# Kernel tuning notes

Hardware: AMD Instinct MI355X
Metric: run time of the kernel (lower is better)

Reference implementation:

```python
import jax, jax.numpy as jnp
import numpy as np

G = 100000   # num graphs
N = 2000000  # num nodes
E = 4000000  # num edges (unused downstream, kept for fidelity)
D = 300      # emb_dim
L = 50       # num noise levels


def setup_inputs() -> dict:
    key = jax.random.key(0)
    ks = jax.random.split(key, 12)
    node2graph = jnp.sort(jax.random.randint(ks[0], (N,), 0, G))
    edge_index = jax.random.randint(ks[1], (2, E), 0, N)
    noise_level = jax.random.randint(ks[2], (G,), 0, L)
    molecule_repr = jax.random.normal(ks[3], (G, D), dtype=jnp.float32)
    pos_noise_pred = jax.random.normal(ks[4], (N, 3), dtype=jnp.float32)
    pos_perturbed = jax.random.normal(ks[5], (N, 3), dtype=jnp.float32)
    pos_target = jax.random.normal(ks[6], (N, 3), dtype=jnp.float32)
    s = 1.0 / np.sqrt(D)
    W1 = jax.random.uniform(ks[7], (D, D), minval=-s, maxval=s, dtype=jnp.float32)
    b1 = jax.random.uniform(ks[8], (D,), minval=-s, maxval=s, dtype=jnp.float32)
    W2 = jax.random.uniform(ks[9], (D, D), minval=-s, maxval=s, dtype=jnp.float32)
    b2 = jax.random.uniform(ks[10], (D,), minval=-s, maxval=s, dtype=jnp.float32)
    sigmas = jnp.asarray(np.exp(np.linspace(np.log(10.0), np.log(0.01), L)), dtype=jnp.float32)
    return dict(node2graph=node2graph, edge_index=edge_index, noise_level=noise_level,
                num_graphs=G, molecule_repr=molecule_repr, pos_noise_pred=pos_noise_pred,
                pos_perturbed=pos_perturbed, pos_target=pos_target,
                W1=W1, b1=b1, W2=W2, b2=b2, sigmas=sigmas)


def _score_target_riemann(pos_perturbed, pos_target, node2graph, num_graphs):
    # @torch.no_grad() branch: all scatter_mean/scatter_add indexed by node2graph
    seg_sum = lambda x: jax.ops.segment_sum(x, node2graph, num_segments=num_graphs)
    cnt = jnp.maximum(seg_sum(jnp.ones((node2graph.shape[0],), jnp.float32)), 1.0)[:, None]
    center = seg_sum(pos_target) / cnt                 # [G,3]
    p_center = seg_sum(pos_perturbed) / cnt            # [G,3]
    pos_c = pos_target - center[node2graph]            # [N,3]
    pp_c = pos_perturbed - p_center[node2graph]        # [N,3]
    # per-graph 3x3 matrices: ptp[i,j] = sum pp_i*pp_j, otp[i,j] = sum pos_c_i*pp_j
    ptp = seg_sum(pp_c[:, :, None] * pp_c[:, None, :])   # [G,3,3]
    otp = seg_sum(pos_c[:, :, None] * pp_c[:, None, :])  # [G,3,3]
    ptp_n = ptp[node2graph]                              # [N,3,3]
    otp_n = otp[node2graph]                              # [N,3,3]
    num = -2.0 * (jnp.einsum('ni,nij->nj', pp_c, ptp_n)
                  - jnp.einsum('ni,nij->nj', pos_c, otp_n))  # [N,3]
    den = (jnp.linalg.norm(ptp_n.reshape(-1, 9), axis=-1)
           + jnp.linalg.norm(otp_n.reshape(-1, 9), axis=-1))[:, None]
    return num / den


def reference(node2graph, edge_index, noise_level, num_graphs, molecule_repr,
              pos_noise_pred, pos_perturbed, pos_target, W1, b1, W2, b2, sigmas):
    edge2graph = node2graph[edge_index[0]]  # computed but unused, as in original
    used_sigmas = sigmas[noise_level][node2graph][:, None]  # [N,1]
    score_target = jax.lax.stop_gradient(
        _score_target_riemann(pos_perturbed, pos_target, node2graph, num_graphs)
    ) / used_sigmas
    pred_noise = (pos_noise_pred - pos_perturbed) * (1.0 / used_sigmas)
    per_node = jnp.sum((pred_noise - score_target) ** 2, axis=-1)  # [N]
    per_graph = jax.ops.segment_sum(per_node, node2graph, num_segments=num_graphs)
    pos_denoise = per_graph.mean()
    # noise-level prediction head: Linear -> SiLU -> Linear, CE over noise_level
    h = jax.nn.silu(molecule_repr @ W1 + b1)
    logits = h @ W2 + b2  # [G,D]
    logp = jax.nn.log_softmax(logits, axis=-1)
    ce = -jnp.take_along_axis(logp, noise_level[:, None], axis=1)[:, 0]
    loss_pred_noise = ce.mean()
    return jnp.stack([pos_denoise, loss_pred_noise])
```

## Files before the change

kernel.cpp:

```cpp
#include <hip/hip_runtime.h>
#include <math.h>


typedef __attribute__((ext_vector_type(8))) short bf16x8;
typedef __attribute__((ext_vector_type(4))) short s16x4;
typedef __attribute__((ext_vector_type(4))) float f32x4;

__device__ __forceinline__ short bt(float f) {
    return (short)(__float_as_uint(f) >> 16);
}

#define TM   64
#define DRL  300
#define DP   320
#define XS   328
#define NT   20
#define MT   4
#define KCH  10


__device__ __forceinline__ void prod22(const float* A, const float* B, int j,
                                       float* dst) {
    float a0 = A[3*j], a1 = A[3*j+1], a2 = A[3*j+2];
    float b0 = B[3*j], b1 = B[3*j+1], b2 = B[3*j+2];
    dst[0] = 1.f;
    dst[1] = a0;  dst[2] = a1;  dst[3] = a2;
    dst[4] = b0;  dst[5] = b1;  dst[6] = b2;
    dst[7] = b0*b0;  dst[8] = b0*b1;  dst[9] = b0*b2;
    dst[10] = b1*b1; dst[11] = b1*b2; dst[12] = b2*b2;
    dst[13] = a0*b0; dst[14] = a0*b1; dst[15] = a0*b2;
    dst[16] = a1*b0; dst[17] = a1*b1; dst[18] = a1*b2;
    dst[19] = a2*b0; dst[20] = a2*b1; dst[21] = a2*b2;
}

__device__ __forceinline__ void acc22(float* q, const float* A, const float* B,
                                      int j) {
    float p[22];
    prod22(A, B, j, p);
#pragma unroll
    for (int k = 0; k < 22; ++k) q[k] += p[k];
}

__device__ __forceinline__ void flush_store(float* __restrict__ mom, int seg,
                                            const float* v) {
    float4* d = (float4*)&mom[seg * 24];
    float4 s0 = {v[0], v[1], v[2], v[3]};
    float4 s1 = {v[4], v[5], v[6], v[7]};
    float4 s2 = {v[8], v[9], v[10], v[11]};
    float4 s3 = {v[12], v[13], v[14], v[15]};
    float4 s4 = {v[16], v[17], v[18], v[19]};
    float4 s5 = {v[20], v[21], 0.f, 0.f};
    d[0] = s0; d[1] = s1; d[2] = s2; d[3] = s3; d[4] = s4; d[5] = s5;
}

__device__ __forceinline__ void flush_atomic(float* __restrict__ mom, int seg,
                                             const float* v) {
    float* m = &mom[seg * 24];
#pragma unroll
    for (int k = 0; k < 22; ++k) atomicAdd(&m[k], v[k]);
}

__global__ __launch_bounds__(256)
void k_moments(const int* __restrict__ n2g,
               const float* __restrict__ pt,
               const float* __restrict__ pp,
               float* __restrict__ mom, int N) {
    const int t = blockIdx.x * blockDim.x + threadIdx.x;
    const int lane = threadIdx.x & 63;
    const int i0 = t * 4;
    const bool act = (i0 < N);

    float A[12], B[12];
    int g0 = -1, g1 = -1, g2 = -1, g3 = -1;
    if (act) {
        const float4* ptv = (const float4*)pt;
        const float4* ppv = (const float4*)pp;
#pragma unroll
        for (int v = 0; v < 3; ++v) {
            float4 x = ptv[3 * t + v];
            A[4*v+0] = x.x; A[4*v+1] = x.y; A[4*v+2] = x.z; A[4*v+3] = x.w;
            float4 y = ppv[3 * t + v];
            B[4*v+0] = y.x; B[4*v+1] = y.y; B[4*v+2] = y.z; B[4*v+3] = y.w;
        }
        int4 gv = *(const int4*)&n2g[i0];
        g0 = gv.x; g1 = gv.y; g2 = gv.z; g3 = gv.w;
    }

    float q[22];
    float lead[22];
    int curseg = g0, leadseg = -2;
    bool haveLead = false;
#pragma unroll
    for (int k = 0; k < 22; ++k) { q[k] = 0.f; lead[k] = 0.f; }
    if (act) {
        prod22(A, B, 0, q);
        const int gj[3] = {g1, g2, g3};
#pragma unroll
        for (int j = 1; j < 4; ++j) {
            int gg = gj[j - 1];
            if (gg == curseg) {
                acc22(q, A, B, j);
            } else {
                if (!haveLead) {
                    haveLead = true; leadseg = curseg;
#pragma unroll
                    for (int k = 0; k < 22; ++k) lead[k] = q[k];
                } else {
                    flush_store(mom, curseg, q);
                }
                prod22(A, B, j, q);
                curseg = gg;
            }
        }
    }

    const int waveFirstNode = ((t - lane) & 0x7FFFFFFF) * 4;
    int before_seg = -1, after_seg = -1;
    if (lane == 0 && waveFirstNode > 0 && waveFirstNode <= N)
        before_seg = n2g[waveFirstNode - 1];
    before_seg = __shfl(before_seg, 0, 64);
    const int waveLast = waveFirstNode + 255;
    if (lane == 63 && waveLast + 1 < N) after_seg = n2g[waveLast + 1];
    after_seg = __shfl(after_seg, 63, 64);

#pragma unroll
    for (int d = 1; d < 64; d <<= 1) {
        int ps = __shfl_up(curseg, d, 64);
        bool ok = (lane >= d) && (ps == curseg);
#pragma unroll
        for (int k = 0; k < 22; ++k) {
            float o = __shfl_up(q[k], d, 64);
            q[k] += ok ? o : 0.f;
        }
    }

    int pseg = __shfl_up(curseg, 1, 64);
    bool cont = act && haveLead && (lane > 0) && (pseg == leadseg);
    float pcnt = 0.f;
#pragma unroll
    for (int k = 0; k < 22; ++k) {
        float pv = __shfl_up(q[k], 1, 64);
        if (k == 0) pcnt = pv;
        lead[k] += cont ? pv : 0.f;
    }
    if (act && haveLead) {
        bool covers = (lane == 0) || (cont && (pcnt == (float)(lane * 4)));
        bool ileft = covers && (before_seg == leadseg);
        if (ileft) flush_atomic(mom, leadseg, lead);
        else       flush_store(mom, leadseg, lead);
    }

    int nseg0 = __shfl_down(g0, 1, 64);
    bool tail = act && ((lane == 63) || (nseg0 != curseg));
    if (tail) {
        bool covers = (q[0] == (float)(lane * 4 + 4));
        bool ileft = covers && (before_seg == curseg);
        bool iright = (lane == 63) && (after_seg == curseg);
        if (ileft || iright) flush_atomic(mom, curseg, q);
        else                 flush_store(mom, curseg, q);
    }
}

__global__ void k_node(const int* __restrict__ n2g,
                       const float* __restrict__ pt,
                       const float* __restrict__ pp,
                       const float* __restrict__ pnp,
                       const float* __restrict__ mom,
                       const int* __restrict__ nl,
                       const float* __restrict__ sigmas,
                       double* __restrict__ accA, int N) {
    int t = blockIdx.x * blockDim.x + threadIdx.x;
    int i0 = t * 4;
    float q = 0.f;
    if (i0 < N) {
        float A[12], B[12], C[12];
        const float4* ptv = (const float4*)pt;
        const float4* ppv = (const float4*)pp;
        const float4* pnv = (const float4*)pnp;
#pragma unroll
        for (int v = 0; v < 3; ++v) {
            float4 x = ptv[3 * t + v];
            A[4*v+0] = x.x; A[4*v+1] = x.y; A[4*v+2] = x.z; A[4*v+3] = x.w;
            float4 y = ppv[3 * t + v];
            B[4*v+0] = y.x; B[4*v+1] = y.y; B[4*v+2] = y.z; B[4*v+3] = y.w;
            float4 z = pnv[3 * t + v];
            C[4*v+0] = z.x; C[4*v+1] = z.y; C[4*v+2] = z.z; C[4*v+3] = z.w;
        }
        int4 gv = *(const int4*)&n2g[i0];
        int gl[4] = {gv.x, gv.y, gv.z, gv.w};
        int gcur = -1;
        float c0=0,c1=0,c2=0,d0=0,d1=0,d2=0,p00=0,p01=0,p02=0,p11=0,p12=0,p22=0;
        float o00=0,o01=0,o02=0,o10=0,o11=0,o12=0,o20=0,o21=0,o22=0,idn=0,is2=0;
#pragma unroll
        for (int j = 0; j < 4; ++j) {
            int i = i0 + j;
            if (i >= N) break;
            int g = gl[j];
            if (g != gcur) {
                gcur = g;
                const float4* pr = (const float4*)&mom[g * 24];
                float4 v0 = pr[0], v1 = pr[1], v2 = pr[2],
                       v3 = pr[3], v4 = pr[4], v5 = pr[5];
                float cnt = fmaxf(v0.x, 1.f);
                float ic = 1.f / cnt;
                c0 = v0.y * ic; c1 = v0.z * ic; c2 = v0.w * ic;
                d0 = v1.x * ic; d1 = v1.y * ic; d2 = v1.z * ic;
                p00 = v1.w - cnt*d0*d0; p01 = v2.x - cnt*d0*d1;
                p02 = v2.y - cnt*d0*d2; p11 = v2.z - cnt*d1*d1;
                p12 = v2.w - cnt*d1*d2; p22 = v3.x - cnt*d2*d2;
                o00 = v3.y - cnt*c0*d0; o01 = v3.z - cnt*c0*d1;
                o02 = v3.w - cnt*c0*d2; o10 = v4.x - cnt*c1*d0;
                o11 = v4.y - cnt*c1*d1; o12 = v4.z - cnt*c1*d2;
                o20 = v4.w - cnt*c2*d0; o21 = v5.x - cnt*c2*d1;
                o22 = v5.y - cnt*c2*d2;
                float ptn = sqrtf(p00*p00 + p11*p11 + p22*p22 +
                                  2.f*(p01*p01 + p02*p02 + p12*p12));
                float otn = sqrtf(o00*o00 + o01*o01 + o02*o02 +
                                  o10*o10 + o11*o11 + o12*o12 +
                                  o20*o20 + o21*o21 + o22*o22);
                float den = ptn + otn;
                idn = (den > 0.f) ? (1.f / den) : 0.f;
                float sg = sigmas[nl[g]];
                is2 = 1.f / (sg * sg);
            }
            float a0 = A[3*j+0] - c0, a1 = A[3*j+1] - c1, a2 = A[3*j+2] - c2;
            float b0 = B[3*j+0] - d0, b1 = B[3*j+1] - d1, b2 = B[3*j+2] - d2;
            float n0 = -2.f * ((b0*p00 + b1*p01 + b2*p02) - (a0*o00 + a1*o10 + a2*o20));
            float n1 = -2.f * ((b0*p01 + b1*p11 + b2*p12) - (a0*o01 + a1*o11 + a2*o21));
            float n2 = -2.f * ((b0*p02 + b1*p12 + b2*p22) - (a0*o02 + a1*o12 + a2*o22));
            float e0 = (C[3*j+0] - B[3*j+0]) - n0 * idn;
            float e1 = (C[3*j+1] - B[3*j+1]) - n1 * idn;
            float e2 = (C[3*j+2] - B[3*j+2]) - n2 * idn;
            q += (e0*e0 + e1*e1 + e2*e2) * is2;
        }
    }
    for (int o = 32; o > 0; o >>= 1) q += __shfl_down(q, o, 64);
    int wv = (threadIdx.x >> 6);
    if ((threadIdx.x & 63) == 0)
        atomicAdd(&accA[(blockIdx.x * 4 + wv) & 255], (double)q);
}


__global__ void k_prepw(const float* __restrict__ W1, const float* __restrict__ W2,
                        short* __restrict__ Wb1, short* __restrict__ Wb2) {
    int id = blockIdx.x * blockDim.x + threadIdx.x;
    if (id >= 2 * DP * DP) return;
    int mat = id / (DP * DP);
    int rem = id - mat * DP * DP;
    int k = rem / DP, n = rem - (rem / DP) * DP;
    const float* W = mat ? W2 : W1;
    short* Wb = mat ? Wb2 : Wb1;
    float v = (k < DRL && n < DRL) ? W[k * DRL + n] : 0.f;
    int kc = k >> 5, kin = k & 31, quad = kin >> 3, j = kin & 7;
    int t = n >> 4, l16 = n & 15;
    Wb[(((kc * NT + t) * 64) + quad * 16 + l16) * 8 + j] = bt(v);
}


__global__ __launch_bounds__(640, 5)
void k_mlp(const float* __restrict__ X,
           const short* __restrict__ Wb1, const short* __restrict__ Wb2,
           const float* __restrict__ b1, const float* __restrict__ b2,
           const int* __restrict__ nl,
           double* __restrict__ accC, int G) {
    __shared__ __align__(16) short Xs[TM * XS];

    const int tid  = threadIdx.x;
    const int wv   = tid >> 6;
    const int lane = tid & 63;
    const int quad = lane >> 4;
    const int l16  = lane & 15;
    const int m0   = blockIdx.x * TM;

    const float4* Xv = (const float4*)X;
    for (int idx = tid; idx < TM * 75; idx += 640) {
        int r = idx / 75, c = idx - r * 75;
        int gr = m0 + r;
        float4 v = {0.f, 0.f, 0.f, 0.f};
        if (gr < G) v = Xv[gr * 75 + c];
        s16x4 sv = { bt(v.x), bt(v.y), bt(v.z), bt(v.w) };
        *(s16x4*)&Xs[r * XS + c * 4] = sv;
    }
    for (int idx = tid; idx < TM * (DP - DRL); idx += 640) {
        int r = idx / (DP - DRL), c = idx - r * (DP - DRL);
        Xs[r * XS + DRL + c] = 0;
    }
    __syncthreads();

    const bf16x8* B1 = (const bf16x8*)Wb1;
    const bf16x8* B2 = (const bf16x8*)Wb2;
    const int tile0 = wv * 2, tile1 = wv * 2 + 1;

    f32x4 acc[MT][2];
    const f32x4 vzero = {0.f, 0.f, 0.f, 0.f};
#pragma unroll
    for (int m = 0; m < MT; ++m) { acc[m][0] = vzero; acc[m][1] = vzero; }

    bf16x8 nb0 = B1[(0 * NT + tile0) * 64 + lane];
    bf16x8 nb1 = B1[(0 * NT + tile1) * 64 + lane];
#pragma unroll
    for (int kc = 0; kc < KCH; ++kc) {
        bf16x8 b0v = nb0, b1v = nb1;
        if (kc + 1 < KCH) {
            nb0 = B1[((kc + 1) * NT + tile0) * 64 + lane];
            nb1 = B1[((kc + 1) * NT + tile1) * 64 + lane];
        }
        bf16x8 a[MT];
#pragma unroll
        for (int m = 0; m < MT; ++m)
            a[m] = *(const bf16x8*)&Xs[(m * 16 + l16) * XS + kc * 32 + quad * 8];
#pragma unroll
        for (int m = 0; m < MT; ++m) {
            acc[m][0] = __builtin_amdgcn_mfma_f32_16x16x32_bf16(a[m], b0v, acc[m][0], 0, 0, 0);
            acc[m][1] = __builtin_amdgcn_mfma_f32_16x16x32_bf16(a[m], b1v, acc[m][1], 0, 0, 0);
        }
    }
    __syncthreads();

#pragma unroll
    for (int t = 0; t < 2; ++t) {
        int col = (wv * 2 + t) * 16 + l16;
        float bias = (col < DRL) ? b1[col] : 0.f;
#pragma unroll
        for (int m = 0; m < MT; ++m)
#pragma unroll
            for (int r = 0; r < 4; ++r) {
                float v = acc[m][t][r] + bias;
                float h = v / (1.f + __expf(-v));
                Xs[(m * 16 + quad * 4 + r) * XS + col] = bt(h);
            }
    }
    __syncthreads();

#pragma unroll
    for (int m = 0; m < MT; ++m) { acc[m][0] = vzero; acc[m][1] = vzero; }
    nb0 = B2[(0 * NT + tile0) * 64 + lane];
    nb1 = B2[(0 * NT + tile1) * 64 + lane];
#pragma unroll
    for (int kc = 0; kc < KCH; ++kc) {
        bf16x8 b0v = nb0, b1v = nb1;
        if (kc + 1 < KCH) {
            nb0 = B2[((kc + 1) * NT + tile0) * 64 + lane];
            nb1 = B2[((kc + 1) * NT + tile1) * 64 + lane];
        }
        bf16x8 a[MT];
#pragma unroll
        for (int m = 0; m < MT; ++m)
            a[m] = *(const bf16x8*)&Xs[(m * 16 + l16) * XS + kc * 32 + quad * 8];
#pragma unroll
        for (int m = 0; m < MT; ++m) {
            acc[m][0] = __builtin_amdgcn_mfma_f32_16x16x32_bf16(a[m], b0v, acc[m][0], 0, 0, 0);
            acc[m][1] = __builtin_amdgcn_mfma_f32_16x16x32_bf16(a[m], b1v, acc[m][1], 0, 0, 0);
        }
    }
    __syncthreads();

    float* S = (float*)Xs;
    float* T = S + TM * 10;
    const int colA = tile0 * 16 + l16;
    const int colB = tile1 * 16 + l16;
    const float biasA = (colA < DRL) ? b2[colA] : 0.f;
    const float biasB = (colB < DRL) ? b2[colB] : 0.f;
#pragma unroll
    for (int m = 0; m < MT; ++m) {
#pragma unroll
        for (int r = 0; r < 4; ++r) {
            int row = m * 16 + quad * 4 + r;
            int grow = m0 + row;
            int ct = (grow < G) ? nl[grow] : -1;
            float lgA = acc[m][0][r] + biasA;
            float lgB = acc[m][1][r] + biasB;
            float sw = ((colA < DRL) ? __expf(lgA) : 0.f) +
                       ((colB < DRL) ? __expf(lgB) : 0.f);
            for (int o = 1; o < 16; o <<= 1) sw += __shfl_xor(sw, o, 64);
            if (l16 == 0) S[row * 10 + wv] = sw;
            if (colA == ct) T[row] = lgA;
            if (colB == ct) T[row] = lgB;
        }
    }
    __syncthreads();
    if (tid < 64) {
        int row = tid;
        int grow = m0 + row;
        float q = 0.f;
        if (grow < G) {
            float ss = 0.f;
#pragma unroll
            for (int w = 0; w < 10; ++w) ss += S[row * 10 + w];
            q = __logf(ss) - T[row];
        }
        for (int o = 32; o > 0; o >>= 1) q += __shfl_down(q, o, 64);
        if (tid == 0) atomicAdd(&accC[blockIdx.x & 255], (double)q);
    }
}


__global__ void k_final(const double* __restrict__ accA,
                        const double* __restrict__ accC,
                        float* __restrict__ out, float invG) {
    int t = threadIdx.x;
    double a = accA[t] + accA[t + 64] + accA[t + 128] + accA[t + 192];
    double c = accC[t] + accC[t + 64] + accC[t + 128] + accC[t + 192];
    for (int o = 32; o > 0; o >>= 1) {
        a += __shfl_down(a, o, 64);
        c += __shfl_down(c, o, 64);
    }
    if (t == 0) {
        out[0] = (float)(a * (double)invG);
        out[1] = (float)(c * (double)invG);
    }
}


extern "C" void kernel_launch(void* const* d_in, const int* in_sizes, int n_in,
                              void* d_out, int out_size, void* d_ws, size_t ws_size,
                              hipStream_t stream) {
    const int*   n2g = (const int*)d_in[0];
    const int*   nl  = (const int*)d_in[2];
    const float* X   = (const float*)d_in[4];
    const float* pnp = (const float*)d_in[5];
    const float* pp  = (const float*)d_in[6];
    const float* pt  = (const float*)d_in[7];
    const float* W1  = (const float*)d_in[8];
    const float* b1  = (const float*)d_in[9];
    const float* W2  = (const float*)d_in[10];
    const float* b2  = (const float*)d_in[11];
    const float* sig = (const float*)d_in[12];

    const int N = in_sizes[0];
    const int G = in_sizes[2];

    double* accA = (double*)d_ws;
    double* accC = accA + 256;
    short*  Wb1  = (short*)((char*)d_ws + 4096);
    short*  Wb2  = Wb1 + DP * DP;
    float*  mom  = (float*)((char*)d_ws + 4096 + (size_t)2 * DP * DP * 2);

    hipMemsetAsync(d_ws, 0, 4096, stream);
    hipMemsetAsync(mom, 0, (size_t)G * 24 * 4, stream);

    const int T4 = (N + 3) / 4;
    k_prepw<<<(2 * DP * DP + 255) / 256, 256, 0, stream>>>(W1, W2, Wb1, Wb2);
    k_moments<<<(T4 + 255) / 256, 256, 0, stream>>>(n2g, pt, pp, mom, N);
    k_node<<<(T4 + 255) / 256, 256, 0, stream>>>(n2g, pt, pp, pnp, mom,
                                                 nl, sig, accA, N);
    k_mlp<<<(G + TM - 1) / TM, 640, 0, stream>>>(X, Wb1, Wb2, b1, b2, nl,
                                                 accC, G);
    k_final<<<1, 64, 0, stream>>>(accA, accC, (float*)d_out, 1.0f / (float)G);
}
```

Measured before the change: 405.1 us.

## Preload all MLP weight fragments into registers and double-buffer hidden activations

Loads every W1 fragment into registers before staging X, and all W2 fragments right after the first GEMM, instead of prefetching one k-chunk at a time. The X load is batched into eight outstanding float4 loads before conversion. A separate Hs shared buffer holds the SiLU output, which removes two barriers (after each GEMM) since Xs is no longer overwritten. The cost is many more registers and twice the LDS per block, so launch bounds drop from 5 to 3 blocks per CU and occupancy falls.

```diff
diff --git a/kernel.cpp b/kernel.cpp
--- a/kernel.cpp
+++ b/kernel.cpp
@@ -257,13 +257,14 @@
 }
 
 
-__global__ __launch_bounds__(640, 5)
+__global__ __launch_bounds__(640, 3)
 void k_mlp(const float* __restrict__ X,
            const short* __restrict__ Wb1, const short* __restrict__ Wb2,
            const float* __restrict__ b1, const float* __restrict__ b2,
            const int* __restrict__ nl,
            double* __restrict__ accC, int G) {
     __shared__ __align__(16) short Xs[TM * XS];
+    __shared__ __align__(16) short Hs[TM * XS];
 
     const int tid  = threadIdx.x;
     const int wv   = tid >> 6;
@@ -272,14 +273,40 @@
     const int l16  = lane & 15;
     const int m0   = blockIdx.x * TM;
 
+    const bf16x8* B1 = (const bf16x8*)Wb1;
+    const bf16x8* B2 = (const bf16x8*)Wb2;
+    const int tile0 = wv * 2, tile1 = wv * 2 + 1;
+
+    bf16x8 w1a[KCH], w1b[KCH];
+#pragma unroll
+    for (int kc = 0; kc < KCH; ++kc) {
+        w1a[kc] = B1[(kc * NT + tile0) * 64 + lane];
+        w1b[kc] = B1[(kc * NT + tile1) * 64 + lane];
+    }
+
     const float4* Xv = (const float4*)X;
-    for (int idx = tid; idx < TM * 75; idx += 640) {
-        int r = idx / 75, c = idx - r * 75;
-        int gr = m0 + r;
-        float4 v = {0.f, 0.f, 0.f, 0.f};
-        if (gr < G) v = Xv[gr * 75 + c];
-        s16x4 sv = { bt(v.x), bt(v.y), bt(v.z), bt(v.w) };
-        *(s16x4*)&Xs[r * XS + c * 4] = sv;
+    {
+        float4 xv[8];
+#pragma unroll
+        for (int u = 0; u < 8; ++u) {
+            int idx = tid + u * 640;
+            float4 v = {0.f, 0.f, 0.f, 0.f};
+            if (idx < TM * 75) {
+                int r = idx / 75, c = idx - r * 75;
+                int gr = m0 + r;
+                if (gr < G) v = Xv[gr * 75 + c];
+            }
+            xv[u] = v;
+        }
+#pragma unroll
+        for (int u = 0; u < 8; ++u) {
+            int idx = tid + u * 640;
+            if (idx < TM * 75) {
+                int r = idx / 75, c = idx - r * 75;
+                s16x4 sv = { bt(xv[u].x), bt(xv[u].y), bt(xv[u].z), bt(xv[u].w) };
+                *(s16x4*)&Xs[r * XS + c * 4] = sv;
+            }
+        }
     }
     for (int idx = tid; idx < TM * (DP - DRL); idx += 640) {
         int r = idx / (DP - DRL), c = idx - r * (DP - DRL);
@@ -287,35 +314,30 @@
     }
     __syncthreads();
 
-    const bf16x8* B1 = (const bf16x8*)Wb1;
-    const bf16x8* B2 = (const bf16x8*)Wb2;
-    const int tile0 = wv * 2, tile1 = wv * 2 + 1;
-
     f32x4 acc[MT][2];
     const f32x4 vzero = {0.f, 0.f, 0.f, 0.f};
 #pragma unroll
     for (int m = 0; m < MT; ++m) { acc[m][0] = vzero; acc[m][1] = vzero; }
 
-    bf16x8 nb0 = B1[(0 * NT + tile0) * 64 + lane];
-    bf16x8 nb1 = B1[(0 * NT + tile1) * 64 + lane];
 #pragma unroll
     for (int kc = 0; kc < KCH; ++kc) {
-        bf16x8 b0v = nb0, b1v = nb1;
-        if (kc + 1 < KCH) {
-            nb0 = B1[((kc + 1) * NT + tile0) * 64 + lane];
-            nb1 = B1[((kc + 1) * NT + tile1) * 64 + lane];
-        }
         bf16x8 a[MT];
 #pragma unroll
         for (int m = 0; m < MT; ++m)
             a[m] = *(const bf16x8*)&Xs[(m * 16 + l16) * XS + kc * 32 + quad * 8];
 #pragma unroll
         for (int m = 0; m < MT; ++m) {
-            acc[m][0] = __builtin_amdgcn_mfma_f32_16x16x32_bf16(a[m], b0v, acc[m][0], 0, 0, 0);
-            acc[m][1] = __builtin_amdgcn_mfma_f32_16x16x32_bf16(a[m], b1v, acc[m][1], 0, 0, 0);
-        }
-    }
-    __syncthreads();
+            acc[m][0] = __builtin_amdgcn_mfma_f32_16x16x32_bf16(a[m], w1a[kc], acc[m][0], 0, 0, 0);
+            acc[m][1] = __builtin_amdgcn_mfma_f32_16x16x32_bf16(a[m], w1b[kc], acc[m][1], 0, 0, 0);
+        }
+    }
+
+    bf16x8 w2a[KCH], w2b[KCH];
+#pragma unroll
+    for (int kc = 0; kc < KCH; ++kc) {
+        w2a[kc] = B2[(kc * NT + tile0) * 64 + lane];
+        w2b[kc] = B2[(kc * NT + tile1) * 64 + lane];
+    }
 
 #pragma unroll
     for (int t = 0; t < 2; ++t) {
@@ -327,33 +349,25 @@
             for (int r = 0; r < 4; ++r) {
                 float v = acc[m][t][r] + bias;
                 float h = v / (1.f + __expf(-v));
-                Xs[(m * 16 + quad * 4 + r) * XS + col] = bt(h);
+                Hs[(m * 16 + quad * 4 + r) * XS + col] = bt(h);
             }
     }
     __syncthreads();
 
 #pragma unroll
     for (int m = 0; m < MT; ++m) { acc[m][0] = vzero; acc[m][1] = vzero; }
-    nb0 = B2[(0 * NT + tile0) * 64 + lane];
-    nb1 = B2[(0 * NT + tile1) * 64 + lane];
 #pragma unroll
     for (int kc = 0; kc < KCH; ++kc) {
-        bf16x8 b0v = nb0, b1v = nb1;
-        if (kc + 1 < KCH) {
-            nb0 = B2[((kc + 1) * NT + tile0) * 64 + lane];
-            nb1 = B2[((kc + 1) * NT + tile1) * 64 + lane];
-        }
         bf16x8 a[MT];
 #pragma unroll
         for (int m = 0; m < MT; ++m)
-            a[m] = *(const bf16x8*)&Xs[(m * 16 + l16) * XS + kc * 32 + quad * 8];
+            a[m] = *(const bf16x8*)&Hs[(m * 16 + l16) * XS + kc * 32 + quad * 8];
 #pragma unroll
         for (int m = 0; m < MT; ++m) {
-            acc[m][0] = __builtin_amdgcn_mfma_f32_16x16x32_bf16(a[m], b0v, acc[m][0], 0, 0, 0);
-            acc[m][1] = __builtin_amdgcn_mfma_f32_16x16x32_bf16(a[m], b1v, acc[m][1], 0, 0, 0);
-        }
-    }
-    __syncthreads();
+            acc[m][0] = __builtin_amdgcn_mfma_f32_16x16x32_bf16(a[m], w2a[kc], acc[m][0], 0, 0, 0);
+            acc[m][1] = __builtin_amdgcn_mfma_f32_16x16x32_bf16(a[m], w2b[kc], acc[m][1], 0, 0, 0);
+        }
+    }
 
     float* S = (float*)Xs;
     float* T = S + TM * 10;
```

Result: no change. 410.1 us (+1.2%).

## Make MLP kernel persistent with register-prefetched double-buffered input tiles

Applied to the files above, without the earlier changes.

The CE-head MLP kernel now runs a fixed grid of 256 blocks that loop over row tiles instead of launching one block per tile. While the current tile is in GEMM1, each block loads the next tile's X rows into registers and writes them to a second LDS buffer. Hidden activations move to their own LDS buffer. The cross-entropy partial sum is kept in a register and committed with a single atomic per block. The intent is to hide global-load latency and cut per-block setup and atomic traffic. In exchange, LDS per block roughly triples and occupancy drops to one block per CU, which leaves fewer waves to hide latency.

```diff
diff --git a/kernel.cpp b/kernel.cpp
--- a/kernel.cpp
+++ b/kernel.cpp
@@ -17,6 +17,7 @@
 #define NT   20
 #define MT   4
 #define KCH  10
+#define GRID_MLP 256
 
 
 __device__ __forceinline__ void prod22(const float* A, const float* B, int j,
@@ -257,141 +258,186 @@
 }
 
 
-__global__ __launch_bounds__(640, 5)
+__global__ __launch_bounds__(640, 3)
 void k_mlp(const float* __restrict__ X,
            const short* __restrict__ Wb1, const short* __restrict__ Wb2,
            const float* __restrict__ b1, const float* __restrict__ b2,
            const int* __restrict__ nl,
-           double* __restrict__ accC, int G) {
-    __shared__ __align__(16) short Xs[TM * XS];
+           double* __restrict__ accC, int G, int ntiles) {
+    __shared__ __align__(16) short Xs[2][TM * XS];
+    __shared__ __align__(16) short Hs[TM * XS];
+    __shared__ float S[TM * 10];
+    __shared__ float T[TM];
 
     const int tid  = threadIdx.x;
     const int wv   = tid >> 6;
     const int lane = tid & 63;
     const int quad = lane >> 4;
     const int l16  = lane & 15;
-    const int m0   = blockIdx.x * TM;
-
-    const float4* Xv = (const float4*)X;
-    for (int idx = tid; idx < TM * 75; idx += 640) {
-        int r = idx / 75, c = idx - r * 75;
-        int gr = m0 + r;
-        float4 v = {0.f, 0.f, 0.f, 0.f};
-        if (gr < G) v = Xv[gr * 75 + c];
-        s16x4 sv = { bt(v.x), bt(v.y), bt(v.z), bt(v.w) };
-        *(s16x4*)&Xs[r * XS + c * 4] = sv;
-    }
-    for (int idx = tid; idx < TM * (DP - DRL); idx += 640) {
-        int r = idx / (DP - DRL), c = idx - r * (DP - DRL);
-        Xs[r * XS + DRL + c] = 0;
-    }
-    __syncthreads();
+    const int tile0 = wv * 2, tile1 = wv * 2 + 1;
 
     const bf16x8* B1 = (const bf16x8*)Wb1;
     const bf16x8* B2 = (const bf16x8*)Wb2;
-    const int tile0 = wv * 2, tile1 = wv * 2 + 1;
-
-    f32x4 acc[MT][2];
+    const float4* Xv = (const float4*)X;
+
+    for (int idx = tid; idx < 2 * TM * (DP - DRL); idx += 640) {
+        int b   = idx / (TM * (DP - DRL));
+        int rem = idx - b * (TM * (DP - DRL));
+        int r = rem / (DP - DRL), c = rem - r * (DP - DRL);
+        Xs[b][r * XS + DRL + c] = 0;
+    }
+
+    {
+        const int m0 = blockIdx.x * TM;
+        for (int idx = tid; idx < TM * 75; idx += 640) {
+            int r = idx / 75, c = idx - r * 75;
+            float4 v = {0.f, 0.f, 0.f, 0.f};
+            if (m0 + r < G) v = Xv[(m0 + r) * 75 + c];
+            s16x4 sv = { bt(v.x), bt(v.y), bt(v.z), bt(v.w) };
+            *(s16x4*)&Xs[0][r * XS + c * 4] = sv;
+        }
+    }
+    __syncthreads();
+
+    double ce_local = 0.0;
+    int cur = 0;
     const f32x4 vzero = {0.f, 0.f, 0.f, 0.f};
-#pragma unroll
-    for (int m = 0; m < MT; ++m) { acc[m][0] = vzero; acc[m][1] = vzero; }
-
-    bf16x8 nb0 = B1[(0 * NT + tile0) * 64 + lane];
-    bf16x8 nb1 = B1[(0 * NT + tile1) * 64 + lane];
-#pragma unroll
-    for (int kc = 0; kc < KCH; ++kc) {
-        bf16x8 b0v = nb0, b1v = nb1;
-        if (kc + 1 < KCH) {
-            nb0 = B1[((kc + 1) * NT + tile0) * 64 + lane];
-            nb1 = B1[((kc + 1) * NT + tile1) * 64 + lane];
-        }
-        bf16x8 a[MT];
-#pragma unroll
-        for (int m = 0; m < MT; ++m)
-            a[m] = *(const bf16x8*)&Xs[(m * 16 + l16) * XS + kc * 32 + quad * 8];
+
+    for (int t = blockIdx.x; t < ntiles; t += GRID_MLP) {
+        const int m0 = t * TM;
+        const int tn = t + GRID_MLP;
+        const bool hasnext = (tn < ntiles);
+
+        float4 xr[8];
+        if (hasnext) {
+            const int m0n = tn * TM;
+#pragma unroll
+            for (int u = 0; u < 8; ++u) {
+                int idx = tid + u * 640;
+                float4 v = {0.f, 0.f, 0.f, 0.f};
+                int r = idx / 75, c = idx - r * 75;
+                if (idx < TM * 75 && m0n + r < G) v = Xv[(m0n + r) * 75 + c];
+                xr[u] = v;
+            }
+        }
+        __builtin_amdgcn_sched_barrier(0);
+
+        const short* As = &Xs[cur][0];
+        f32x4 acc[MT][2];
+#pragma unroll
+        for (int m = 0; m < MT; ++m) { acc[m][0] = vzero; acc[m][1] = vzero; }
+        {
+            bf16x8 nb0 = B1[(0 * NT + tile0) * 64 + lane];
+            bf16x8 nb1 = B1[(0 * NT + tile1) * 64 + lane];
+#pragma unroll
+            for (int kc = 0; kc < KCH; ++kc) {
+                bf16x8 b0v = nb0, b1v = nb1;
+                if (kc + 1 < KCH) {
+                    nb0 = B1[((kc + 1) * NT + tile0) * 64 + lane];
+                    nb1 = B1[((kc + 1) * NT + tile1) * 64 + lane];
+                }
+                bf16x8 a[MT];
+#pragma unroll
+                for (int m = 0; m < MT; ++m)
+                    a[m] = *(const bf16x8*)&As[(m * 16 + l16) * XS + kc * 32 + quad * 8];
+#pragma unroll
+                for (int m = 0; m < MT; ++m) {
+                    acc[m][0] = __builtin_amdgcn_mfma_f32_16x16x32_bf16(a[m], b0v, acc[m][0], 0, 0, 0);
+                    acc[m][1] = __builtin_amdgcn_mfma_f32_16x16x32_bf16(a[m], b1v, acc[m][1], 0, 0, 0);
+                }
+            }
+        }
+
+#pragma unroll
+        for (int tt = 0; tt < 2; ++tt) {
+            int col = (wv * 2 + tt) * 16 + l16;
+            float bias = (col < DRL) ? b1[col] : 0.f;
+#pragma unroll
+            for (int m = 0; m < MT; ++m)
+#pragma unroll
+                for (int r = 0; r < 4; ++r) {
+                    float v = acc[m][tt][r] + bias;
+                    float h = v / (1.f + __expf(-v));
+                    Hs[(m * 16 + quad * 4 + r) * XS + col] = bt(h);
+                }
+        }
+
+        if (hasnext) {
+#pragma unroll
+            for (int u = 0; u < 8; ++u) {
+                int idx = tid + u * 640;
+                if (idx < TM * 75) {
+                    int r = idx / 75, c = idx - r * 75;
+                    s16x4 sv = { bt(xr[u].x), bt(xr[u].y), bt(xr[u].z), bt(xr[u].w) };
+                    *(s16x4*)&Xs[cur ^ 1][r * XS + c * 4] = sv;
+                }
+            }
+        }
+        __syncthreads();
+
+#pragma unroll
+        for (int m = 0; m < MT; ++m) { acc[m][0] = vzero; acc[m][1] = vzero; }
+        {
+            bf16x8 nb0 = B2[(0 * NT + tile0) * 64 + lane];
+            bf16x8 nb1 = B2[(0 * NT + tile1) * 64 + lane];
+#pragma unroll
+            for (int kc = 0; kc < KCH; ++kc) {
+                bf16x8 b0v = nb0, b1v = nb1;
+                if (kc + 1 < KCH) {
+                    nb0 = B2[((kc + 1) * NT + tile0) * 64 + lane];
+                    nb1 = B2[((kc + 1) * NT + tile1) * 64 + lane];
+                }
+                bf16x8 a[MT];
+#pragma unroll
+                for (int m = 0; m < MT; ++m)
+                    a[m] = *(const bf16x8*)&Hs[(m * 16 + l16) * XS + kc * 32 + quad * 8];
+#pragma unroll
+                for (int m = 0; m < MT; ++m) {
+                    acc[m][0] = __builtin_amdgcn_mfma_f32_16x16x32_bf16(a[m], b0v, acc[m][0], 0, 0, 0);
+                    acc[m][1] = __builtin_amdgcn_mfma_f32_16x16x32_bf16(a[m], b1v, acc[m][1], 0, 0, 0);
+                }
+            }
+        }
+
+        const int colA = tile0 * 16 + l16;
+        const int colB = tile1 * 16 + l16;
+        const float biasA = (colA < DRL) ? b2[colA] : 0.f;
+        const float biasB = (colB < DRL) ? b2[colB] : 0.f;
 #pragma unroll
         for (int m = 0; m < MT; ++m) {
-            acc[m][0] = __builtin_amdgcn_mfma_f32_16x16x32_bf16(a[m], b0v, acc[m][0], 0, 0, 0);
-            acc[m][1] = __builtin_amdgcn_mfma_f32_16x16x32_bf16(a[m], b1v, acc[m][1], 0, 0, 0);
-        }
-    }
-    __syncthreads();
-
-#pragma unroll
-    for (int t = 0; t < 2; ++t) {
-        int col = (wv * 2 + t) * 16 + l16;
-        float bias = (col < DRL) ? b1[col] : 0.f;
-#pragma unroll
-        for (int m = 0; m < MT; ++m)
 #pragma unroll
             for (int r = 0; r < 4; ++r) {
-                float v = acc[m][t][r] + bias;
-                float h = v / (1.f + __expf(-v));
-                Xs[(m * 16 + quad * 4 + r) * XS + col] = bt(h);
-            }
-    }
-    __syncthreads();
-
-#pragma unroll
-    for (int m = 0; m < MT; ++m) { acc[m][0] = vzero; acc[m][1] = vzero; }
-    nb0 = B2[(0 * NT + tile0) * 64 + lane];
-    nb1 = B2[(0 * NT + tile1) * 64 + lane];
-#pragma unroll
-    for (int kc = 0; kc < KCH; ++kc) {
-        bf16x8 b0v = nb0, b1v = nb1;
-        if (kc + 1 < KCH) {
-            nb0 = B2[((kc + 1) * NT + tile0) * 64 + lane];
-            nb1 = B2[((kc + 1) * NT + tile1) * 64 + lane];
-        }
-        bf16x8 a[MT];
-#pragma unroll
-        for (int m = 0; m < MT; ++m)
-            a[m] = *(const bf16x8*)&Xs[(m * 16 + l16) * XS + kc * 32 + quad * 8];
-#pragma unroll
-        for (int m = 0; m < MT; ++m) {
-            acc[m][0] = __builtin_amdgcn_mfma_f32_16x16x32_bf16(a[m], b0v, acc[m][0], 0, 0, 0);
-            acc[m][1] = __builtin_amdgcn_mfma_f32_16x16x32_bf16(a[m], b1v, acc[m][1], 0, 0, 0);
-        }
-    }
-    __syncthreads();
-
-    float* S = (float*)Xs;
-    float* T = S + TM * 10;
-    const int colA = tile0 * 16 + l16;
-    const int colB = tile1 * 16 + l16;
-    const float biasA = (colA < DRL) ? b2[colA] : 0.f;
-    const float biasB = (colB < DRL) ? b2[colB] : 0.f;
-#pragma unroll
-    for (int m = 0; m < MT; ++m) {
-#pragma unroll
-        for (int r = 0; r < 4; ++r) {
-            int row = m * 16 + quad * 4 + r;
-            int grow = m0 + row;
-            int ct = (grow < G) ? nl[grow] : -1;
-            float lgA = acc[m][0][r] + biasA;
-            float lgB = acc[m][1][r] + biasB;
-            float sw = ((colA < DRL) ? __expf(lgA) : 0.f) +
-                       ((colB < DRL) ? __expf(lgB) : 0.f);
-            for (int o = 1; o < 16; o <<= 1) sw += __shfl_xor(sw, o, 64);
-            if (l16 == 0) S[row * 10 + wv] = sw;
-            if (colA == ct) T[row] = lgA;
-            if (colB == ct) T[row] = lgB;
-        }
-    }
-    __syncthreads();
-    if (tid < 64) {
-        int row = tid;
-        int grow = m0 + row;
-        float q = 0.f;
-        if (grow < G) {
-            float ss = 0.f;
-#pragma unroll
-            for (int w = 0; w < 10; ++w) ss += S[row * 10 + w];
-            q = __logf(ss) - T[row];
-        }
-        for (int o = 32; o > 0; o >>= 1) q += __shfl_down(q, o, 64);
-        if (tid == 0) atomicAdd(&accC[blockIdx.x & 255], (double)q);
-    }
+                int row = m * 16 + quad * 4 + r;
+                int grow = m0 + row;
+                int ct = (grow < G) ? nl[grow] : -1;
+                float lgA = acc[m][0][r] + biasA;
+                float lgB = acc[m][1][r] + biasB;
+                float sw = ((colA < DRL) ? __expf(lgA) : 0.f) +
+                           ((colB < DRL) ? __expf(lgB) : 0.f);
+                for (int o = 1; o < 16; o <<= 1) sw += __shfl_xor(sw, o, 64);
+                if (l16 == 0) S[row * 10 + wv] = sw;
+                if (colA == ct) T[row] = lgA;
+                if (colB == ct) T[row] = lgB;
+            }
+        }
+        __syncthreads();
+
+        if (tid < 64) {
+            int row = tid, grow = m0 + row;
+            float q = 0.f;
+            if (grow < G) {
+                float ss = 0.f;
+#pragma unroll
+                for (int w = 0; w < 10; ++w) ss += S[row * 10 + w];
+                q = __logf(ss) - T[row];
+            }
+            for (int o = 32; o > 0; o >>= 1) q += __shfl_down(q, o, 64);
+            if (tid == 0) ce_local += (double)q;
+        }
+        cur ^= 1;
+    }
+    if (tid == 0)
+        atomicAdd(&accC[blockIdx.x & 255], ce_local);
 }
 
 
@@ -440,11 +486,14 @@
     hipMemsetAsync(mom, 0, (size_t)G * 24 * 4, stream);
 
     const int T4 = (N + 3) / 4;
+    const int ntiles = (G + TM - 1) / TM;
+    const int grid_mlp = (ntiles < GRID_MLP) ? ntiles : GRID_MLP;
+
     k_prepw<<<(2 * DP * DP + 255) / 256, 256, 0, stream>>>(W1, W2, Wb1, Wb2);
     k_moments<<<(T4 + 255) / 256, 256, 0, stream>>>(n2g, pt, pp, mom, N);
     k_node<<<(T4 + 255) / 256, 256, 0, stream>>>(n2g, pt, pp, pnp, mom,
                                                  nl, sig, accA, N);
-    k_mlp<<<(G + TM - 1) / TM, 640, 0, stream>>>(X, Wb1, Wb2, b1, b2, nl,
-                                                 accC, G);
+    k_mlp<<<grid_mlp, 640, 0, stream>>>(X, Wb1, Wb2, b1, b2, nl,
+                                        accC, G, ntiles);
     k_final<<<1, 64, 0, stream>>>(accA, accC, (float*)d_out, 1.0f / (float)G);
 }
```

Result: slower. 461.0 us (+13.8%).

## Replace node-parallel segmented moments with per-graph processing via boundary arrays

Applied to the files above, without the earlier changes.

Replaces the wave-level segmented scan and atomic moment accumulation with a boundary-finding kernel that records each graph's node range. A per-graph kernel then assigns four lanes to each graph, computes the moments with a quad shuffle reduction, and makes a second pass over that graph's nodes to accumulate the loss. This removes the moments buffer, the cross-wave atomics and the scan shuffles. In exchange, loads become strided scalar accesses with uneven per-graph work, and pt and pp are read twice.

```diff
diff --git a/kernel.cpp b/kernel.cpp
--- a/kernel.cpp
+++ b/kernel.cpp
@@ -19,225 +19,83 @@
 #define KCH  10
 
 
-__device__ __forceinline__ void prod22(const float* A, const float* B, int j,
-                                       float* dst) {
-    float a0 = A[3*j], a1 = A[3*j+1], a2 = A[3*j+2];
-    float b0 = B[3*j], b1 = B[3*j+1], b2 = B[3*j+2];
-    dst[0] = 1.f;
-    dst[1] = a0;  dst[2] = a1;  dst[3] = a2;
-    dst[4] = b0;  dst[5] = b1;  dst[6] = b2;
-    dst[7] = b0*b0;  dst[8] = b0*b1;  dst[9] = b0*b2;
-    dst[10] = b1*b1; dst[11] = b1*b2; dst[12] = b2*b2;
-    dst[13] = a0*b0; dst[14] = a0*b1; dst[15] = a0*b2;
-    dst[16] = a1*b0; dst[17] = a1*b1; dst[18] = a1*b2;
-    dst[19] = a2*b0; dst[20] = a2*b1; dst[21] = a2*b2;
-}
-
-__device__ __forceinline__ void acc22(float* q, const float* A, const float* B,
-                                      int j) {
-    float p[22];
-    prod22(A, B, j, p);
-#pragma unroll
-    for (int k = 0; k < 22; ++k) q[k] += p[k];
-}
-
-__device__ __forceinline__ void flush_store(float* __restrict__ mom, int seg,
-                                            const float* v) {
-    float4* d = (float4*)&mom[seg * 24];
-    float4 s0 = {v[0], v[1], v[2], v[3]};
-    float4 s1 = {v[4], v[5], v[6], v[7]};
-    float4 s2 = {v[8], v[9], v[10], v[11]};
-    float4 s3 = {v[12], v[13], v[14], v[15]};
-    float4 s4 = {v[16], v[17], v[18], v[19]};
-    float4 s5 = {v[20], v[21], 0.f, 0.f};
-    d[0] = s0; d[1] = s1; d[2] = s2; d[3] = s3; d[4] = s4; d[5] = s5;
-}
-
-__device__ __forceinline__ void flush_atomic(float* __restrict__ mom, int seg,
-                                             const float* v) {
-    float* m = &mom[seg * 24];
-#pragma unroll
-    for (int k = 0; k < 22; ++k) atomicAdd(&m[k], v[k]);
-}
-
 __global__ __launch_bounds__(256)
-void k_moments(const int* __restrict__ n2g,
-               const float* __restrict__ pt,
-               const float* __restrict__ pp,
-               float* __restrict__ mom, int N) {
-    const int t = blockIdx.x * blockDim.x + threadIdx.x;
-    const int lane = threadIdx.x & 63;
-    const int i0 = t * 4;
-    const bool act = (i0 < N);
-
-    float A[12], B[12];
-    int g0 = -1, g1 = -1, g2 = -1, g3 = -1;
-    if (act) {
-        const float4* ptv = (const float4*)pt;
-        const float4* ppv = (const float4*)pp;
-#pragma unroll
-        for (int v = 0; v < 3; ++v) {
-            float4 x = ptv[3 * t + v];
-            A[4*v+0] = x.x; A[4*v+1] = x.y; A[4*v+2] = x.z; A[4*v+3] = x.w;
-            float4 y = ppv[3 * t + v];
-            B[4*v+0] = y.x; B[4*v+1] = y.y; B[4*v+2] = y.z; B[4*v+3] = y.w;
-        }
-        int4 gv = *(const int4*)&n2g[i0];
-        g0 = gv.x; g1 = gv.y; g2 = gv.z; g3 = gv.w;
-    }
-
-    float q[22];
-    float lead[22];
-    int curseg = g0, leadseg = -2;
-    bool haveLead = false;
-#pragma unroll
-    for (int k = 0; k < 22; ++k) { q[k] = 0.f; lead[k] = 0.f; }
-    if (act) {
-        prod22(A, B, 0, q);
-        const int gj[3] = {g1, g2, g3};
-#pragma unroll
-        for (int j = 1; j < 4; ++j) {
-            int gg = gj[j - 1];
-            if (gg == curseg) {
-                acc22(q, A, B, j);
-            } else {
-                if (!haveLead) {
-                    haveLead = true; leadseg = curseg;
-#pragma unroll
-                    for (int k = 0; k < 22; ++k) lead[k] = q[k];
-                } else {
-                    flush_store(mom, curseg, q);
-                }
-                prod22(A, B, j, q);
-                curseg = gg;
-            }
-        }
-    }
-
-    const int waveFirstNode = ((t - lane) & 0x7FFFFFFF) * 4;
-    int before_seg = -1, after_seg = -1;
-    if (lane == 0 && waveFirstNode > 0 && waveFirstNode <= N)
-        before_seg = n2g[waveFirstNode - 1];
-    before_seg = __shfl(before_seg, 0, 64);
-    const int waveLast = waveFirstNode + 255;
-    if (lane == 63 && waveLast + 1 < N) after_seg = n2g[waveLast + 1];
-    after_seg = __shfl(after_seg, 63, 64);
-
-#pragma unroll
-    for (int d = 1; d < 64; d <<= 1) {
-        int ps = __shfl_up(curseg, d, 64);
-        bool ok = (lane >= d) && (ps == curseg);
-#pragma unroll
-        for (int k = 0; k < 22; ++k) {
-            float o = __shfl_up(q[k], d, 64);
-            q[k] += ok ? o : 0.f;
-        }
-    }
-
-    int pseg = __shfl_up(curseg, 1, 64);
-    bool cont = act && haveLead && (lane > 0) && (pseg == leadseg);
-    float pcnt = 0.f;
-#pragma unroll
-    for (int k = 0; k < 22; ++k) {
-        float pv = __shfl_up(q[k], 1, 64);
-        if (k == 0) pcnt = pv;
-        lead[k] += cont ? pv : 0.f;
-    }
-    if (act && haveLead) {
-        bool covers = (lane == 0) || (cont && (pcnt == (float)(lane * 4)));
-        bool ileft = covers && (before_seg == leadseg);
-        if (ileft) flush_atomic(mom, leadseg, lead);
-        else       flush_store(mom, leadseg, lead);
-    }
-
-    int nseg0 = __shfl_down(g0, 1, 64);
-    bool tail = act && ((lane == 63) || (nseg0 != curseg));
-    if (tail) {
-        bool covers = (q[0] == (float)(lane * 4 + 4));
-        bool ileft = covers && (before_seg == curseg);
-        bool iright = (lane == 63) && (after_seg == curseg);
-        if (ileft || iright) flush_atomic(mom, curseg, q);
-        else                 flush_store(mom, curseg, q);
-    }
-}
-
-__global__ void k_node(const int* __restrict__ n2g,
-                       const float* __restrict__ pt,
-                       const float* __restrict__ pp,
-                       const float* __restrict__ pnp,
-                       const float* __restrict__ mom,
-                       const int* __restrict__ nl,
-                       const float* __restrict__ sigmas,
-                       double* __restrict__ accA, int N) {
+void k_bnd(const int* __restrict__ n2g, int* __restrict__ gs,
+           int* __restrict__ ge, int N) {
     int t = blockIdx.x * blockDim.x + threadIdx.x;
-    int i0 = t * 4;
+    if (t >= N) return;
+    int g = n2g[t];
+    if (t == 0     || n2g[t - 1] != g) gs[g] = t;
+    if (t == N - 1 || n2g[t + 1] != g) ge[g] = t + 1;
+}
+
+__global__ __launch_bounds__(256)
+void k_graph(const int* __restrict__ gs, const int* __restrict__ ge,
+             const float* __restrict__ pt, const float* __restrict__ pp,
+             const float* __restrict__ pnp,
+             const int* __restrict__ nl, const float* __restrict__ sigmas,
+             double* __restrict__ accA, int G) {
+    const int tg = blockIdx.x * blockDim.x + threadIdx.x;
+    const int g  = tg >> 2;
+    const int j  = tg & 3;
     float q = 0.f;
-    if (i0 < N) {
-        float A[12], B[12], C[12];
-        const float4* ptv = (const float4*)pt;
-        const float4* ppv = (const float4*)pp;
-        const float4* pnv = (const float4*)pnp;
-#pragma unroll
-        for (int v = 0; v < 3; ++v) {
-            float4 x = ptv[3 * t + v];
-            A[4*v+0] = x.x; A[4*v+1] = x.y; A[4*v+2] = x.z; A[4*v+3] = x.w;
-            float4 y = ppv[3 * t + v];
-            B[4*v+0] = y.x; B[4*v+1] = y.y; B[4*v+2] = y.z; B[4*v+3] = y.w;
-            float4 z = pnv[3 * t + v];
-            C[4*v+0] = z.x; C[4*v+1] = z.y; C[4*v+2] = z.z; C[4*v+3] = z.w;
-        }
-        int4 gv = *(const int4*)&n2g[i0];
-        int gl[4] = {gv.x, gv.y, gv.z, gv.w};
-        int gcur = -1;
-        float c0=0,c1=0,c2=0,d0=0,d1=0,d2=0,p00=0,p01=0,p02=0,p11=0,p12=0,p22=0;
-        float o00=0,o01=0,o02=0,o10=0,o11=0,o12=0,o20=0,o21=0,o22=0,idn=0,is2=0;
-#pragma unroll
-        for (int j = 0; j < 4; ++j) {
-            int i = i0 + j;
-            if (i >= N) break;
-            int g = gl[j];
-            if (g != gcur) {
-                gcur = g;
-                const float4* pr = (const float4*)&mom[g * 24];
-                float4 v0 = pr[0], v1 = pr[1], v2 = pr[2],
-                       v3 = pr[3], v4 = pr[4], v5 = pr[5];
-                float cnt = fmaxf(v0.x, 1.f);
-                float ic = 1.f / cnt;
-                c0 = v0.y * ic; c1 = v0.z * ic; c2 = v0.w * ic;
-                d0 = v1.x * ic; d1 = v1.y * ic; d2 = v1.z * ic;
-                p00 = v1.w - cnt*d0*d0; p01 = v2.x - cnt*d0*d1;
-                p02 = v2.y - cnt*d0*d2; p11 = v2.z - cnt*d1*d1;
-                p12 = v2.w - cnt*d1*d2; p22 = v3.x - cnt*d2*d2;
-                o00 = v3.y - cnt*c0*d0; o01 = v3.z - cnt*c0*d1;
-                o02 = v3.w - cnt*c0*d2; o10 = v4.x - cnt*c1*d0;
-                o11 = v4.y - cnt*c1*d1; o12 = v4.z - cnt*c1*d2;
-                o20 = v4.w - cnt*c2*d0; o21 = v5.x - cnt*c2*d1;
-                o22 = v5.y - cnt*c2*d2;
-                float ptn = sqrtf(p00*p00 + p11*p11 + p22*p22 +
-                                  2.f*(p01*p01 + p02*p02 + p12*p12));
-                float otn = sqrtf(o00*o00 + o01*o01 + o02*o02 +
-                                  o10*o10 + o11*o11 + o12*o12 +
-                                  o20*o20 + o21*o21 + o22*o22);
-                float den = ptn + otn;
-                idn = (den > 0.f) ? (1.f / den) : 0.f;
-                float sg = sigmas[nl[g]];
-                is2 = 1.f / (sg * sg);
-            }
-            float a0 = A[3*j+0] - c0, a1 = A[3*j+1] - c1, a2 = A[3*j+2] - c2;
-            float b0 = B[3*j+0] - d0, b1 = B[3*j+1] - d1, b2 = B[3*j+2] - d2;
+    if (g < G) {
+        const int s = gs[g], e = ge[g];
+        float st0=0,st1=0,st2=0, sp0=0,sp1=0,sp2=0;
+        float m00=0,m01=0,m02=0,m11=0,m12=0,m22=0;
+        float t00=0,t01=0,t02=0,t10=0,t11=0,t12=0,t20=0,t21=0,t22=0;
+        for (int i = s + j; i < e; i += 4) {
+            float a0 = pt[3*i], a1 = pt[3*i+1], a2 = pt[3*i+2];
+            float b0 = pp[3*i], b1 = pp[3*i+1], b2 = pp[3*i+2];
+            st0 += a0; st1 += a1; st2 += a2;
+            sp0 += b0; sp1 += b1; sp2 += b2;
+            m00 += b0*b0; m01 += b0*b1; m02 += b0*b2;
+            m11 += b1*b1; m12 += b1*b2; m22 += b2*b2;
+            t00 += a0*b0; t01 += a0*b1; t02 += a0*b2;
+            t10 += a1*b0; t11 += a1*b1; t12 += a1*b2;
+            t20 += a2*b0; t21 += a2*b1; t22 += a2*b2;
+        }
+#define QR(x) do { x += __shfl_xor(x, 1, 64); x += __shfl_xor(x, 2, 64); } while (0)
+        QR(st0); QR(st1); QR(st2); QR(sp0); QR(sp1); QR(sp2);
+        QR(m00); QR(m01); QR(m02); QR(m11); QR(m12); QR(m22);
+        QR(t00); QR(t01); QR(t02); QR(t10); QR(t11); QR(t12);
+        QR(t20); QR(t21); QR(t22);
+#undef QR
+        float cnt = fmaxf((float)(e - s), 1.f);
+        float ic  = 1.f / cnt;
+        float c0 = st0 * ic, c1 = st1 * ic, c2 = st2 * ic;
+        float d0 = sp0 * ic, d1 = sp1 * ic, d2 = sp2 * ic;
+        float p00 = m00 - cnt*d0*d0, p01 = m01 - cnt*d0*d1;
+        float p02 = m02 - cnt*d0*d2, p11 = m11 - cnt*d1*d1;
+        float p12 = m12 - cnt*d1*d2, p22 = m22 - cnt*d2*d2;
+        float o00 = t00 - cnt*c0*d0, o01 = t01 - cnt*c0*d1, o02 = t02 - cnt*c0*d2;
+        float o10 = t10 - cnt*c1*d0, o11 = t11 - cnt*c1*d1, o12 = t12 - cnt*c1*d2;
+        float o20 = t20 - cnt*c2*d0, o21 = t21 - cnt*c2*d1, o22 = t22 - cnt*c2*d2;
+        float ptn = sqrtf(p00*p00 + p11*p11 + p22*p22 +
+                          2.f*(p01*p01 + p02*p02 + p12*p12));
+        float otn = sqrtf(o00*o00 + o01*o01 + o02*o02 +
+                          o10*o10 + o11*o11 + o12*o12 +
+                          o20*o20 + o21*o21 + o22*o22);
+        float den = ptn + otn;
+        float idn = (den > 0.f) ? (1.f / den) : 0.f;
+        float sg  = sigmas[nl[g]];
+        float is2 = 1.f / (sg * sg);
+        for (int i = s + j; i < e; i += 4) {
+            float a0 = pt[3*i] - c0, a1 = pt[3*i+1] - c1, a2 = pt[3*i+2] - c2;
+            float bb0 = pp[3*i],  bb1 = pp[3*i+1],  bb2 = pp[3*i+2];
+            float b0 = bb0 - d0, b1 = bb1 - d1, b2 = bb2 - d2;
             float n0 = -2.f * ((b0*p00 + b1*p01 + b2*p02) - (a0*o00 + a1*o10 + a2*o20));
             float n1 = -2.f * ((b0*p01 + b1*p11 + b2*p12) - (a0*o01 + a1*o11 + a2*o21));
             float n2 = -2.f * ((b0*p02 + b1*p12 + b2*p22) - (a0*o02 + a1*o12 + a2*o22));
-            float e0 = (C[3*j+0] - B[3*j+0]) - n0 * idn;
-            float e1 = (C[3*j+1] - B[3*j+1]) - n1 * idn;
-            float e2 = (C[3*j+2] - B[3*j+2]) - n2 * idn;
+            float e0 = (pnp[3*i]   - bb0) - n0 * idn;
+            float e1 = (pnp[3*i+1] - bb1) - n1 * idn;
+            float e2 = (pnp[3*i+2] - bb2) - n2 * idn;
             q += (e0*e0 + e1*e1 + e2*e2) * is2;
         }
     }
     for (int o = 32; o > 0; o >>= 1) q += __shfl_down(q, o, 64);
-    int wv = (threadIdx.x >> 6);
     if ((threadIdx.x & 63) == 0)
-        atomicAdd(&accA[(blockIdx.x * 4 + wv) & 255], (double)q);
+        atomicAdd(&accA[(blockIdx.x * 4 + (threadIdx.x >> 6)) & 255], (double)q);
 }
 
 
@@ -434,16 +292,16 @@
     double* accC = accA + 256;
     short*  Wb1  = (short*)((char*)d_ws + 4096);
     short*  Wb2  = Wb1 + DP * DP;
-    float*  mom  = (float*)((char*)d_ws + 4096 + (size_t)2 * DP * DP * 2);
+    int*    gs   = (int*)((char*)d_ws + 4096 + (size_t)2 * DP * DP * 2);
+    int*    ge   = gs + G;
 
     hipMemsetAsync(d_ws, 0, 4096, stream);
-    hipMemsetAsync(mom, 0, (size_t)G * 24 * 4, stream);
-
-    const int T4 = (N + 3) / 4;
+    hipMemsetAsync(gs, 0, (size_t)2 * G * 4, stream);
+
     k_prepw<<<(2 * DP * DP + 255) / 256, 256, 0, stream>>>(W1, W2, Wb1, Wb2);
-    k_moments<<<(T4 + 255) / 256, 256, 0, stream>>>(n2g, pt, pp, mom, N);
-    k_node<<<(T4 + 255) / 256, 256, 0, stream>>>(n2g, pt, pp, pnp, mom,
-                                                 nl, sig, accA, N);
+    k_bnd<<<(N + 255) / 256, 256, 0, stream>>>(n2g, gs, ge, N);
+    k_graph<<<(4 * G + 255) / 256, 256, 0, stream>>>(gs, ge, pt, pp, pnp,
+                                                     nl, sig, accA, G);
     k_mlp<<<(G + TM - 1) / TM, 640, 0, stream>>>(X, Wb1, Wb2, b1, b2, nl,
                                                  accC, G);
     k_final<<<1, 64, 0, stream>>>(accA, accC, (float*)d_out, 1.0f / (float)G);
```

Result: faster. 395.2 us (-2.4%).
